# Kernel optimization log

Hardware: AMD Instinct MI355X
Metric: run time of the kernel (lower is better)

Reference implementation:

```python
import jax, jax.numpy as jnp
import numpy as np

B, T, E, H = 2, 2048, 1024, 16  # batch, seq(block_size), n_embed, n_head


def setup_inputs() -> dict:
    key = jax.random.key(0)
    kx, kq, kk, kv, kf = jax.random.split(key, 5)
    s = 0.02
    return {
        "x": jax.random.normal(kx, (B, T, E), jnp.float32),
        "Wq": jax.random.normal(kq, (E, E), jnp.float32) * s,
        "Wk": jax.random.normal(kk, (E, E), jnp.float32) * s,
        "Wv": jax.random.normal(kv, (E, E), jnp.float32) * s,
        "Wf": jax.random.normal(kf, (E, E), jnp.float32) * s,
        "bf": jnp.zeros((E,), jnp.float32),
    }


def reference(x, Wq, Wk, Wv, Wf, bf):
    b, t, e = x.shape
    dh = e // H
    # per-head projections (no bias), heads concatenated along feature dim
    q = (x @ Wq).reshape(b, t, H, dh)
    k = (x @ Wk).reshape(b, t, H, dh)
    v = (x @ Wv).reshape(b, t, H, dh)
    # NOTE: original scales by sqrt(full embed dim C), not sqrt(head_size)
    scores = jnp.einsum("bqhd,bkhd->bhqk", q, k) / jnp.sqrt(jnp.asarray(e, x.dtype))
    causal = jnp.tril(jnp.ones((t, t), bool))
    scores = jnp.where(causal, scores, -jnp.inf)
    wei = jax.nn.softmax(scores, axis=-1)
    attn = jnp.einsum("bhqk,bkhd->bqhd", wei, v).reshape(b, t, e)
    x = x + attn  # residual (no out-projection in original)
    # FeedForward: single Linear + ReLU, residual
    return x + jnp.maximum(x @ Wf + bf, 0)
```

## Files before the change

### kernel.cpp

```cpp
#include <hip/hip_runtime.h>
#include <cstdint>
#include <cstddef>

typedef unsigned short u16;
typedef short short8 __attribute__((ext_vector_type(8)));
typedef float floatx4 __attribute__((ext_vector_type(4)));

__device__ __forceinline__ float bf2f(u16 u) {
    union { unsigned int i; float f; } v; v.i = ((unsigned int)u) << 16; return v.f;
}
__device__ __forceinline__ u16 f2bf(float f) {
    union { float f; unsigned int i; } v; v.f = f;
    unsigned int u = v.i;
    return (u16)((u + 0x7fffu + ((u >> 16) & 1u)) >> 16);
}

#if __has_builtin(__builtin_amdgcn_exp2f)
#define EXP2F(x) __builtin_amdgcn_exp2f(x)
#else
#define EXP2F(x) exp2f(x)
#endif

__device__ __forceinline__ void gload_lds16(const u16* g, void* lds_wave_base) {
    __builtin_amdgcn_global_load_lds(
        (__attribute__((address_space(1))) void*)g,
        (__attribute__((address_space(3))) void*)lds_wave_base,
        16, 0, 0);
}

__global__ void conv_transpose_k(const float* __restrict__ w0, const float* __restrict__ w1,
                                 const float* __restrict__ w2, const float* __restrict__ w3,
                                 u16* __restrict__ o0, u16* __restrict__ o1,
                                 u16* __restrict__ o2, u16* __restrict__ o3, int n) {
    __shared__ float t[32][33];
    const float* w; u16* o;
    switch (blockIdx.z) {
        case 0: w = w0; o = o0; break;
        case 1: w = w1; o = o1; break;
        case 2: w = w2; o = o2; break;
        default: w = w3; o = o3; break;
    }
    int tx = threadIdx.x, ty = threadIdx.y;
    int x0 = blockIdx.x * 32, y0 = blockIdx.y * 32;
    t[ty][tx] = w[(size_t)(y0 + ty) * n + x0 + tx];
    __syncthreads();
    o[(size_t)(x0 + ty) * n + y0 + tx] = f2bf(t[tx][ty]);
}

__global__ void conv_k(const float* __restrict__ in, u16* __restrict__ out, int n) {
    int i = (blockIdx.x * blockDim.x + threadIdx.x) * 4;
    if (i >= n) return;
    float4 v = *(const float4*)&in[i];
    ushort4 o;
    o.x = f2bf(v.x); o.y = f2bf(v.y); o.z = f2bf(v.z); o.w = f2bf(v.w);
    *(ushort4*)&out[i] = o;
}

__global__ void vpack_k(const u16* __restrict__ vbd, u16* __restrict__ vp, int T) {
    __shared__ u16 t[32][33];
    int bh = blockIdx.z;
    int t0 = blockIdx.x * 32, d0 = blockIdx.y * 32;
    int tx = threadIdx.x, ty = threadIdx.y;
    t[ty][tx] = vbd[((size_t)bh * T + t0 + ty) * 64 + d0 + tx];
    __syncthreads();
    int kblk = t0 >> 6, tbase = t0 & 32;
    vp[(((size_t)bh * (T / 64) + kblk) * 64 + d0 + ty) * 64 + tbase + tx] = t[tx][ty];
}

__global__ __launch_bounds__(256) void gemm_qkv(
    const u16* __restrict__ A, const u16* __restrict__ Bt,
    u16* __restrict__ qpk, u16* __restrict__ kpk, u16* __restrict__ vbd,
    int M, int T, int K) {
    __shared__ u16 lds_a[128][32];
    __shared__ u16 lds_b[128][32];

    const int tid = threadIdx.x;
    const int lane = tid & 63, wave = tid >> 6;
    const int wm = (wave >> 1) * 64, wn = (wave & 1) * 64;
    const int bm = blockIdx.x * 128, bn = blockIdx.y * 128;
    const int l15 = lane & 15, lq = lane >> 4;

    const int sec = bn >> 10;
    u16* dst = (sec == 0) ? qpk : (sec == 1) ? kpk : vbd;
    const int bnE = bn & 1023;

    floatx4 acc[4][4];
#pragma unroll
    for (int i = 0; i < 4; ++i)
#pragma unroll
        for (int j = 0; j < 4; ++j) acc[i][j] = (floatx4)0.0f;

    for (int k0 = 0; k0 < K; k0 += 32) {
#pragma unroll
        for (int it = 0; it < 2; ++it) {
            int idx = it * 256 + tid;
            int row = idx >> 2;
            int c8 = (idx & 3) * 8;
            size_t ldsoff = (size_t)(it * 256 + wave * 64) * 16;
            gload_lds16(&A[(size_t)(bm + row) * K + k0 + c8], (char*)&lds_a[0][0] + ldsoff);
            gload_lds16(&Bt[(size_t)(bn + row) * K + k0 + c8], (char*)&lds_b[0][0] + ldsoff);
        }
        __syncthreads();

        short8 af[4], bfr[4];
#pragma unroll
        for (int i = 0; i < 4; ++i) af[i] = *(const short8*)&lds_a[wm + i * 16 + l15][lq * 8];
#pragma unroll
        for (int j = 0; j < 4; ++j) bfr[j] = *(const short8*)&lds_b[wn + j * 16 + l15][lq * 8];

#pragma unroll
        for (int i = 0; i < 4; ++i)
#pragma unroll
            for (int j = 0; j < 4; ++j)
                acc[i][j] = __builtin_amdgcn_mfma_f32_16x16x32_bf16(af[i], bfr[j], acc[i][j], 0, 0, 0);
        __syncthreads();
    }

#pragma unroll
    for (int i = 0; i < 4; ++i)
#pragma unroll
        for (int j = 0; j < 4; ++j)
#pragma unroll
            for (int r = 0; r < 4; ++r) {
                int row = bm + wm + i * 16 + lq * 4 + r;
                int colE = bnE + wn + j * 16 + l15;
                int h = colE >> 6, d = colE & 63;
                int b = row >> 11, t = row & 2047;
                dst[(((size_t)(b * 16 + h) * T) + t) * 64 + d] = f2bf(acc[i][j][r]);
            }
}

__global__ __launch_bounds__(256) void gemm64_bt(
    const u16* __restrict__ A, const u16* __restrict__ Bt, float* __restrict__ Cf,
    const float* __restrict__ bias, const u16* __restrict__ resid,
    int M, int N, int K) {
    __shared__ u16 lds_a[64][32];
    __shared__ u16 lds_b[128][32];

    const int tid = threadIdx.x;
    const int lane = tid & 63, wave = tid >> 6;
    const int wm = (wave >> 1) * 32, wn = (wave & 1) * 64;
    const int bm = blockIdx.x * 64, bn = blockIdx.y * 128;
    const int l15 = lane & 15, lq = lane >> 4;

    floatx4 acc[2][4];
#pragma unroll
    for (int i = 0; i < 2; ++i)
#pragma unroll
        for (int j = 0; j < 4; ++j) acc[i][j] = (floatx4)0.0f;

    for (int k0 = 0; k0 < K; k0 += 32) {
        {
            int row = tid >> 2;
            int c8 = (tid & 3) * 8;
            size_t ldsoff = (size_t)(wave * 64) * 16;
            gload_lds16(&A[(size_t)(bm + row) * K + k0 + c8], (char*)&lds_a[0][0] + ldsoff);
        }
#pragma unroll
        for (int it = 0; it < 2; ++it) {
            int idx = it * 256 + tid;
            int row = idx >> 2;
            int c8 = (idx & 3) * 8;
            size_t ldsoff = (size_t)(it * 256 + wave * 64) * 16;
            gload_lds16(&Bt[(size_t)(bn + row) * K + k0 + c8], (char*)&lds_b[0][0] + ldsoff);
        }
        __syncthreads();

        short8 af[2], bfr[4];
#pragma unroll
        for (int i = 0; i < 2; ++i) af[i] = *(const short8*)&lds_a[wm + i * 16 + l15][lq * 8];
#pragma unroll
        for (int j = 0; j < 4; ++j) bfr[j] = *(const short8*)&lds_b[wn + j * 16 + l15][lq * 8];

#pragma unroll
        for (int i = 0; i < 2; ++i)
#pragma unroll
            for (int j = 0; j < 4; ++j)
                acc[i][j] = __builtin_amdgcn_mfma_f32_16x16x32_bf16(af[i], bfr[j], acc[i][j], 0, 0, 0);
        __syncthreads();
    }

#pragma unroll
    for (int i = 0; i < 2; ++i)
#pragma unroll
        for (int j = 0; j < 4; ++j)
#pragma unroll
            for (int r = 0; r < 4; ++r) {
                int row = bm + wm + i * 16 + lq * 4 + r;
                int col = bn + wn + j * 16 + l15;
                float v = acc[i][j][r];
                v = fmaxf(v + bias[col], 0.0f) + bf2f(resid[(size_t)row * N + col]);
                Cf[(size_t)row * N + col] = v;
            }
}

#define STAGE(KT, BUF)                                                            \
    {                                                                             \
        const u16* kc_ = kb + (size_t)((KT) * 64 + r0) * 64 + swz0;               \
        gload_lds16(kc_, (char*)kbuf + (BUF) * 8192 + wave * 1024);               \
        gload_lds16(kc_ + 32 * 64, (char*)kbuf + (BUF) * 8192 + 4096 + wave * 1024); \
        const u16* vc_ = vp + (size_t)(KT) * 4096 + r0 * 64 + swz0;               \
        gload_lds16(vc_, (char*)vbuf + (BUF) * 8192 + wave * 1024);               \
        gload_lds16(vc_ + 32 * 64, (char*)vbuf + (BUF) * 8192 + 4096 + wave * 1024); \
    }

__global__ __launch_bounds__(256) void attn9_k(
    const u16* __restrict__ qpk, const u16* __restrict__ kpk,
    const u16* __restrict__ vpack, const float* __restrict__ xf,
    u16* __restrict__ y, int T, int E) {
    __shared__ u16 kbuf[2][64 * 64];
    __shared__ u16 vbuf[2][64 * 64];
    __shared__ u16 lds_p[4][16][72];

    const int tid = threadIdx.x;
    const int lane = tid & 63, wave = tid >> 6;
    const int l15 = lane & 15, lq = lane >> 4;
    const int bh = blockIdx.x;
    const int b = bh >> 4, h = bh & 15;
    const int bx = blockIdx.y;

    const u16* qp = qpk + (size_t)bh * T * 64;
    const u16* kb = kpk + (size_t)bh * T * 64;
    const u16* vp = vpack + (size_t)bh * T * 64;

    const float c2 = 0.04508422f;
    const int r0 = tid >> 3;
    const int slot = tid & 7;
    const int swz0 = ((slot - (r0 & 7)) & 7) * 8;
    const int fsw = (l15 & 7) * 16;

#pragma unroll 1
    for (int p = 0; p < 2; ++p) {
        const int qb = p ? (31 - bx) : bx;
        const int qt = qb * 64 + wave * 16;
        const int nkb = qb + 1;

        short8 aq[2];
#pragma unroll
        for (int c = 0; c < 2; ++c)
            aq[c] = *(const short8*)&qp[(size_t)(qt + l15) * 64 + c * 32 + lq * 8];

        floatx4 o[4];
#pragma unroll
        for (int n = 0; n < 4; ++n) o[n] = (floatx4)0.0f;
        float lsum[4];
#pragma unroll
        for (int r = 0; r < 4; ++r) lsum[r] = 0.0f;

        STAGE(0, 0);
        __syncthreads();

#pragma unroll 1
        for (int kt = 0; kt < nkb; ++kt) {
            const int kc0 = kt * 64;
            const int cur = kt & 1;
            const int curoff = cur * 8192;

            if (kt + 1 < nkb) STAGE(kt + 1, cur ^ 1);

            floatx4 s[4];
#pragma unroll
            for (int t2 = 0; t2 < 4; ++t2) {
                floatx4 sa = (floatx4)0.0f;
#pragma unroll
                for (int c = 0; c < 2; ++c) {
                    int off = (t2 * 16 + l15) * 128 + ((c * 64 + lq * 16 + fsw) & 127);
                    short8 bk = *(const short8*)((const char*)kbuf + curoff + off);
                    sa = __builtin_amdgcn_mfma_f32_16x16x32_bf16(aq[c], bk, sa, 0, 0, 0);
                }
                s[t2] = sa;
            }

            const bool partial = (kt == qb);
#pragma unroll
            for (int t2 = 0; t2 < 4; ++t2)
#pragma unroll
                for (int r = 0; r < 4; ++r) {
                    float pv;
                    if (partial) {
                        int colg = kc0 + t2 * 16 + l15;
                        int rowg = qt + lq * 4 + r;
                        pv = (colg <= rowg) ? EXP2F(s[t2][r] * c2) : 0.0f;
                    } else {
                        pv = EXP2F(s[t2][r] * c2);
                    }
                    lsum[r] += pv;
                    lds_p[wave][lq * 4 + r][t2 * 16 + l15] = f2bf(pv);
                }

#pragma unroll
            for (int kc = 0; kc < 2; ++kc) {
                short8 ap = *(const short8*)&lds_p[wave][l15][kc * 32 + lq * 8];
#pragma unroll
                for (int n = 0; n < 4; ++n) {
                    int off = (n * 16 + l15) * 128 + ((kc * 64 + lq * 16 + fsw) & 127);
                    short8 bv = *(const short8*)((const char*)vbuf + curoff + off);
                    o[n] = __builtin_amdgcn_mfma_f32_16x16x32_bf16(ap, bv, o[n], 0, 0, 0);
                }
            }
            __syncthreads();
        }

#pragma unroll
        for (int r = 0; r < 4; ++r) {
#pragma unroll
            for (int msk = 1; msk < 16; msk <<= 1) lsum[r] += __shfl_xor(lsum[r], msk, 64);
        }
        const float* xp = xf + (size_t)b * T * E + (size_t)h * 64;
        u16* yp = y + (size_t)b * T * E + (size_t)h * 64;
        float rl[4];
#pragma unroll
        for (int r = 0; r < 4; ++r) rl[r] = 1.0f / lsum[r];
#pragma unroll
        for (int n = 0; n < 4; ++n)
#pragma unroll
            for (int r = 0; r < 4; ++r) {
                int rowg = qt + lq * 4 + r;
                int col = n * 16 + l15;
                float val = o[n][r] * rl[r];
                float res = __builtin_nontemporal_load(xp + (size_t)rowg * E + col);
                yp[(size_t)rowg * E + col] = f2bf(res + val);
            }
    }
}

extern "C" void kernel_launch(void* const* d_in, const int* in_sizes, int n_in,
                              void* d_out, int out_size, void* d_ws, size_t ws_size,
                              hipStream_t stream) {
    const int B = 2, T = 2048, E = 1024;
    const int M = B * T;

    const float* x  = (const float*)d_in[0];
    const float* Wq = (const float*)d_in[1];
    const float* Wk = (const float*)d_in[2];
    const float* Wv = (const float*)d_in[3];
    const float* Wf = (const float*)d_in[4];
    const float* bf = (const float*)d_in[5];
    float* out = (float*)d_out;

    u16* ws = (u16*)d_ws;
    const size_t WN = (size_t)E * E;
    const size_t XN = (size_t)M * E;
    u16* Wqkv  = ws;
    u16* WfT   = ws + 3 * WN;
    u16* xb    = ws + 4 * WN;
    u16* qpk   = ws + 4 * WN + XN;
    u16* kpk   = ws + 4 * WN + 2 * XN;
    u16* vbd   = ws + 4 * WN + 3 * XN;
    u16* yb    = ws + 4 * WN + 4 * XN;
    u16* vpack = xb;

    conv_transpose_k<<<dim3(E / 32, E / 32, 4), dim3(32, 32), 0, stream>>>(
        Wq, Wk, Wv, Wf, Wqkv, Wqkv + WN, Wqkv + 2 * WN, WfT, E);
    conv_k<<<(int)(XN / 1024), 256, 0, stream>>>(x, xb, (int)XN);

    gemm_qkv<<<dim3(M / 128, 3 * E / 128), 256, 0, stream>>>(
        xb, Wqkv, qpk, kpk, vbd, M, T, E);

    vpack_k<<<dim3(T / 32, 2, B * 16), dim3(32, 32), 0, stream>>>(vbd, vpack, T);

    attn9_k<<<dim3(B * 16, T / 64 / 2), 256, 0, stream>>>(qpk, kpk, vpack, x, yb, T, E);

    gemm64_bt<<<dim3(M / 64, E / 128), 256, 0, stream>>>(yb, WfT, out, bf, yb, M, E, E);
}
```

Measured before the change: 205.5 us.

## Keep attention P in registers via transposed QK^T MFMA, one query block per workgroup

The attention kernel now computes S^T by swapping the MFMA operands, so each lane's exponentiated scores line up with the A-operand layout of the PV MFMA. It packs them with v_cvt_pk_bf16_f32 and feeds them straight from registers, removing the per-tile LDS round trip for P. The K/V LDS swizzle is changed to match the new read pattern. The row-sum reduction becomes two shuffles plus a broadcast. The grid doubles to one query block per workgroup, launched heaviest-first, instead of pairing light and heavy blocks per workgroup, which trades paired load balancing for more parallelism and depends on the hardware scheduler.

```diff
diff --git a/kernel.cpp b/kernel.cpp
--- a/kernel.cpp
+++ b/kernel.cpp
@@ -204,20 +204,19 @@
         gload_lds16(vc_ + 32 * 64, (char*)vbuf + (BUF) * 8192 + 4096 + wave * 1024); \
     }
 
-__global__ __launch_bounds__(256) void attn9_k(
+__global__ __launch_bounds__(256) void attn10_k(
     const u16* __restrict__ qpk, const u16* __restrict__ kpk,
     const u16* __restrict__ vpack, const float* __restrict__ xf,
     u16* __restrict__ y, int T, int E) {
     __shared__ u16 kbuf[2][64 * 64];
     __shared__ u16 vbuf[2][64 * 64];
-    __shared__ u16 lds_p[4][16][72];
 
     const int tid = threadIdx.x;
     const int lane = tid & 63, wave = tid >> 6;
     const int l15 = lane & 15, lq = lane >> 4;
     const int bh = blockIdx.x;
     const int b = bh >> 4, h = bh & 15;
-    const int bx = blockIdx.y;
+    const int qb = 31 - (int)blockIdx.y;
 
     const u16* qp = qpk + (size_t)bh * T * 64;
     const u16* kb = kpk + (size_t)bh * T * 64;
@@ -226,102 +225,112 @@
     const float c2 = 0.04508422f;
     const int r0 = tid >> 3;
     const int slot = tid & 7;
-    const int swz0 = ((slot - (r0 & 7)) & 7) * 8;
-    const int fsw = (l15 & 7) * 16;
+    const int fr0 = (r0 & 3) | (((r0 >> 3) & 1) << 2);
+    const int swz0 = ((slot - fr0) & 7) * 8;
+
+    const int rbase = ((l15 >> 2) * 8) + (l15 & 3);
+    const int sA = lq + (l15 & 7);
+    const int sB = lq + ((l15 & 3) | (((l15 >> 3) & 1) << 2));
+
+    const int qt = qb * 64 + wave * 16;
+    const int qg = qt + l15;
+    const int nkb = qb + 1;
+
+    short8 aq[2];
+#pragma unroll
+    for (int c = 0; c < 2; ++c)
+        aq[c] = *(const short8*)&qp[(size_t)qg * 64 + c * 32 + lq * 8];
+
+    floatx4 o[4];
+#pragma unroll
+    for (int n = 0; n < 4; ++n) o[n] = (floatx4)0.0f;
+    float lsum = 0.0f;
+
+    STAGE(0, 0);
+    __syncthreads();
 
 #pragma unroll 1
-    for (int p = 0; p < 2; ++p) {
-        const int qb = p ? (31 - bx) : bx;
-        const int qt = qb * 64 + wave * 16;
-        const int nkb = qb + 1;
-
-        short8 aq[2];
-#pragma unroll
-        for (int c = 0; c < 2; ++c)
-            aq[c] = *(const short8*)&qp[(size_t)(qt + l15) * 64 + c * 32 + lq * 8];
-
-        floatx4 o[4];
-#pragma unroll
-        for (int n = 0; n < 4; ++n) o[n] = (floatx4)0.0f;
-        float lsum[4];
-#pragma unroll
-        for (int r = 0; r < 4; ++r) lsum[r] = 0.0f;
-
-        STAGE(0, 0);
-        __syncthreads();
-
-#pragma unroll 1
-        for (int kt = 0; kt < nkb; ++kt) {
-            const int kc0 = kt * 64;
-            const int cur = kt & 1;
-            const int curoff = cur * 8192;
-
-            if (kt + 1 < nkb) STAGE(kt + 1, cur ^ 1);
-
-            floatx4 s[4];
-#pragma unroll
-            for (int t2 = 0; t2 < 4; ++t2) {
-                floatx4 sa = (floatx4)0.0f;
-#pragma unroll
-                for (int c = 0; c < 2; ++c) {
-                    int off = (t2 * 16 + l15) * 128 + ((c * 64 + lq * 16 + fsw) & 127);
-                    short8 bk = *(const short8*)((const char*)kbuf + curoff + off);
-                    sa = __builtin_amdgcn_mfma_f32_16x16x32_bf16(aq[c], bk, sa, 0, 0, 0);
-                }
-                s[t2] = sa;
-            }
-
-            const bool partial = (kt == qb);
-#pragma unroll
-            for (int t2 = 0; t2 < 4; ++t2)
-#pragma unroll
-                for (int r = 0; r < 4; ++r) {
-                    float pv;
-                    if (partial) {
-                        int colg = kc0 + t2 * 16 + l15;
-                        int rowg = qt + lq * 4 + r;
-                        pv = (colg <= rowg) ? EXP2F(s[t2][r] * c2) : 0.0f;
-                    } else {
-                        pv = EXP2F(s[t2][r] * c2);
-                    }
-                    lsum[r] += pv;
-                    lds_p[wave][lq * 4 + r][t2 * 16 + l15] = f2bf(pv);
-                }
-
-#pragma unroll
-            for (int kc = 0; kc < 2; ++kc) {
-                short8 ap = *(const short8*)&lds_p[wave][l15][kc * 32 + lq * 8];
-#pragma unroll
-                for (int n = 0; n < 4; ++n) {
-                    int off = (n * 16 + l15) * 128 + ((kc * 64 + lq * 16 + fsw) & 127);
-                    short8 bv = *(const short8*)((const char*)vbuf + curoff + off);
-                    o[n] = __builtin_amdgcn_mfma_f32_16x16x32_bf16(ap, bv, o[n], 0, 0, 0);
-                }
-            }
-            __syncthreads();
-        }
-
+    for (int kt = 0; kt < nkb; ++kt) {
+        const int kc0 = kt * 64;
+        const int cur = kt & 1;
+        const int curoff = cur * 8192;
+
+        if (kt + 1 < nkb) STAGE(kt + 1, cur ^ 1);
+
+        floatx4 st[4];
+#pragma unroll
+        for (int t2 = 0; t2 < 4; ++t2) {
+            const int row = rbase + (t2 & 1) * 4 + (t2 >> 1) * 32;
+            floatx4 sa = (floatx4)0.0f;
+#pragma unroll
+            for (int c = 0; c < 2; ++c) {
+                int off = row * 128 + ((c * 4 + sA) & 7) * 16;
+                short8 bk = *(const short8*)((const char*)kbuf + curoff + off);
+                sa = __builtin_amdgcn_mfma_f32_16x16x32_bf16(bk, aq[c], sa, 0, 0, 0);
+            }
+            st[t2] = sa;
+        }
+
+        const bool partial = (kt == qb);
+        unsigned int pw[8];
+#pragma unroll
+        for (int t2 = 0; t2 < 4; ++t2) {
+            float e0, e1, e2, e3;
+            const int kg0 = kc0 + lq * 8 + (t2 & 1) * 4 + ((t2 >> 1) * 32);
+            if (partial) {
+                e0 = (kg0 + 0 <= qg) ? EXP2F(st[t2][0] * c2) : 0.0f;
+                e1 = (kg0 + 1 <= qg) ? EXP2F(st[t2][1] * c2) : 0.0f;
+                e2 = (kg0 + 2 <= qg) ? EXP2F(st[t2][2] * c2) : 0.0f;
+                e3 = (kg0 + 3 <= qg) ? EXP2F(st[t2][3] * c2) : 0.0f;
+            } else {
+                e0 = EXP2F(st[t2][0] * c2);
+                e1 = EXP2F(st[t2][1] * c2);
+                e2 = EXP2F(st[t2][2] * c2);
+                e3 = EXP2F(st[t2][3] * c2);
+            }
+            lsum += (e0 + e1) + (e2 + e3);
+            unsigned int w0, w1;
+            asm("v_cvt_pk_bf16_f32 %0, %1, %2" : "=v"(w0) : "v"(e0), "v"(e1));
+            asm("v_cvt_pk_bf16_f32 %0, %1, %2" : "=v"(w1) : "v"(e2), "v"(e3));
+            pw[t2 * 2 + 0] = w0;
+            pw[t2 * 2 + 1] = w1;
+        }
+
+#pragma unroll
+        for (int kc = 0; kc < 2; ++kc) {
+            union { unsigned int u[4]; short8 s; } ap;
+            ap.u[0] = pw[kc * 4 + 0];
+            ap.u[1] = pw[kc * 4 + 1];
+            ap.u[2] = pw[kc * 4 + 2];
+            ap.u[3] = pw[kc * 4 + 3];
+#pragma unroll
+            for (int n = 0; n < 4; ++n) {
+                int off = (n * 16 + l15) * 128 + ((kc * 4 + sB) & 7) * 16;
+                short8 bv = *(const short8*)((const char*)vbuf + curoff + off);
+                o[n] = __builtin_amdgcn_mfma_f32_16x16x32_bf16(ap.s, bv, o[n], 0, 0, 0);
+            }
+        }
+        __syncthreads();
+    }
+
+    lsum += __shfl_xor(lsum, 16, 64);
+    lsum += __shfl_xor(lsum, 32, 64);
+
+    const float* xp = xf + (size_t)b * T * E + (size_t)h * 64;
+    u16* yp = y + (size_t)b * T * E + (size_t)h * 64;
+    float rl[4];
+#pragma unroll
+    for (int r = 0; r < 4; ++r) rl[r] = 1.0f / __shfl(lsum, lq * 4 + r, 64);
+#pragma unroll
+    for (int n = 0; n < 4; ++n)
 #pragma unroll
         for (int r = 0; r < 4; ++r) {
-#pragma unroll
-            for (int msk = 1; msk < 16; msk <<= 1) lsum[r] += __shfl_xor(lsum[r], msk, 64);
-        }
-        const float* xp = xf + (size_t)b * T * E + (size_t)h * 64;
-        u16* yp = y + (size_t)b * T * E + (size_t)h * 64;
-        float rl[4];
-#pragma unroll
-        for (int r = 0; r < 4; ++r) rl[r] = 1.0f / lsum[r];
-#pragma unroll
-        for (int n = 0; n < 4; ++n)
-#pragma unroll
-            for (int r = 0; r < 4; ++r) {
-                int rowg = qt + lq * 4 + r;
-                int col = n * 16 + l15;
-                float val = o[n][r] * rl[r];
-                float res = __builtin_nontemporal_load(xp + (size_t)rowg * E + col);
-                yp[(size_t)rowg * E + col] = f2bf(res + val);
-            }
-    }
+            int rowg = qt + lq * 4 + r;
+            int col = n * 16 + l15;
+            float val = o[n][r] * rl[r];
+            float res = __builtin_nontemporal_load(xp + (size_t)rowg * E + col);
+            yp[(size_t)rowg * E + col] = f2bf(res + val);
+        }
 }
 
 extern "C" void kernel_launch(void* const* d_in, const int* in_sizes, int n_in,
@@ -359,7 +368,7 @@
 
     vpack_k<<<dim3(T / 32, 2, B * 16), dim3(32, 32), 0, stream>>>(vbd, vpack, T);
 
-    attn9_k<<<dim3(B * 16, T / 64 / 2), 256, 0, stream>>>(qpk, kpk, vpack, x, yb, T, E);
+    attn10_k<<<dim3(B * 16, T / 64), 256, 0, stream>>>(qpk, kpk, vpack, x, yb, T, E);
 
     gemm64_bt<<<dim3(M / 64, E / 128), 256, 0, stream>>>(yb, WfT, out, bf, yb, M, E, E);
 }
```

Result: faster. 193.1 us (-6.0%).
